# Kernel tuning notes

Hardware: AMD Instinct MI355X
Metric: run time of the kernel (lower is better)

Reference implementation:

```python
import jax, jax.numpy as jnp
import numpy as np

VOCAB, D, H, L, SEQ = 32000, 768, 12, 6, 1024
HD = D // H
DFF = 4 * D
EPS = 1e-5


def _ln(x, g, b):
    mu = jnp.mean(x, axis=-1, keepdims=True)
    var = jnp.var(x, axis=-1, keepdims=True)
    return (x - mu) * jax.lax.rsqrt(var + EPS) * g + b


def setup_inputs() -> dict:
    key = jax.random.key(0)
    ks = jax.random.split(key, 10)
    s = lambda *sh: 0.02
    return {
        "idx": jax.random.randint(ks[0], (2, SEQ), 0, VOCAB, dtype=jnp.int64) if jax.config.jax_enable_x64 else jax.random.randint(ks[0], (2, SEQ), 0, VOCAB, dtype=jnp.int32),
        "tok_emb": jax.random.normal(ks[1], (VOCAB, D), jnp.float32) * 0.02,
        "pos_emb": jax.random.normal(ks[2], (SEQ, D), jnp.float32) * 0.02,
        "Wqkv": jax.random.normal(ks[3], (L, D, 3 * D), jnp.float32) * 0.02,
        "bqkv": jnp.zeros((L, 3 * D), jnp.float32),
        "Wo": jax.random.normal(ks[4], (L, D, D), jnp.float32) * 0.02,
        "bo": jnp.zeros((L, D), jnp.float32),
        "ln1_g": jnp.ones((L, D), jnp.float32),
        "ln1_b": jnp.zeros((L, D), jnp.float32),
        "ln2_g": jnp.ones((L, D), jnp.float32),
        "ln2_b": jnp.zeros((L, D), jnp.float32),
        "W1": jax.random.normal(ks[5], (L, D, DFF), jnp.float32) * 0.02,
        "b1": jnp.zeros((L, DFF), jnp.float32),
        "W2": jax.random.normal(ks[6], (L, DFF, D), jnp.float32) * 0.02,
        "b2": jnp.zeros((L, D), jnp.float32),
        "lnf_g": jnp.ones((D,), jnp.float32),
        "lnf_b": jnp.zeros((D,), jnp.float32),
        "Wlm": jax.random.normal(ks[7], (D, VOCAB), jnp.float32) * 0.02,
    }


def _forward(idx, tok_emb, pos_emb, Wqkv, bqkv, Wo, bo, ln1_g, ln1_b,
             ln2_g, ln2_b, W1, b1, W2, b2, lnf_g, lnf_b, Wlm):
    B, T = idx.shape
    x = tok_emb[idx] + pos_emb[None, :T]  # [B,T,D]
    causal = jnp.tril(jnp.ones((T, T), bool))  # [T,T]
    for l in range(L):
        h = _ln(x, ln1_g[l], ln1_b[l])
        qkv = h @ Wqkv[l] + bqkv[l]  # [B,T,3D]
        qkv = qkv.reshape(B, T, 3, H, HD).transpose(2, 0, 3, 1, 4)
        q, k, v = qkv[0], qkv[1], qkv[2]  # each [B,H,T,HD]
        att = jnp.einsum('bhqd,bhkd->bhqk', q, k) / np.sqrt(HD).astype(np.float32)
        att = jnp.where(causal, att, -jnp.inf)
        att = jax.nn.softmax(att, axis=-1)
        o = jnp.einsum('bhqk,bhkd->bhqd', att, v)
        o = o.transpose(0, 2, 1, 3).reshape(B, T, D)
        x = x + o @ Wo[l] + bo[l]
        h = _ln(x, ln2_g[l], ln2_b[l])
        x = x + jax.nn.gelu(h @ W1[l] + b1[l], approximate=False) @ W2[l] + b2[l]
    x = _ln(x, lnf_g, lnf_b)
    return x @ Wlm  # [B,T,VOCAB]


def reference(idx, tok_emb, pos_emb, Wqkv, bqkv, Wo, bo, ln1_g, ln1_b,
              ln2_g, ln2_b, W1, b1, W2, b2, lnf_g, lnf_b, Wlm):
    return _forward(idx, tok_emb, pos_emb, Wqkv, bqkv, Wo, bo, ln1_g, ln1_b,
                    ln2_g, ln2_b, W1, b1, W2, b2, lnf_g, lnf_b, Wlm)
```

## Files before the change

### kernel.cpp

```cpp
#include <hip/hip_runtime.h>
#include <math.h>

#define TT   1024
#define DD   768
#define HH   12
#define LLAY 6
#define DFFN 3072
#define BB   2
#define NTOK (BB*TT)

typedef __bf16 bf16;
typedef __attribute__((ext_vector_type(8))) __bf16 bf16x8;
typedef __attribute__((ext_vector_type(4))) __bf16 bf16x4;
typedef __attribute__((ext_vector_type(4))) float f32x4;

__device__ inline unsigned pack_bf16x2(float a, float b) {
    union { bf16 h[2]; unsigned u; } un;
    un.h[0] = (bf16)a; un.h[1] = (bf16)b;
    return un.u;
}

__device__ inline void gload16(const bf16* g, bf16* l) {
    __builtin_amdgcn_global_load_lds((const void*)g, (void*)l, 16, 0, 0);
}

template<int N> __device__ inline void waitcnt_vm() {
    if constexpr (N == 0) asm volatile("s_waitcnt vmcnt(0)" ::: "memory");
    else if constexpr (N == 3) asm volatile("s_waitcnt vmcnt(3)" ::: "memory");
    else if constexpr (N == 4) asm volatile("s_waitcnt vmcnt(4)" ::: "memory");
}

__global__ __launch_bounds__(256) void embed_kernel(const int* __restrict__ idx,
                                                    const float* __restrict__ tok,
                                                    const float* __restrict__ pos,
                                                    float* __restrict__ x) {
    int bt = blockIdx.x;
    int t  = bt % TT;
    int id = idx[bt];
    const float* te = tok + (size_t)id * DD;
    const float* pe = pos + (size_t)t * DD;
    float* xr = x + (size_t)bt * DD;
    for (int d = threadIdx.x; d < DD; d += 256) xr[d] = te[d] + pe[d];
}

__global__ __launch_bounds__(256) void ln_kernel(const float* __restrict__ in,
                                                 const float* __restrict__ g,
                                                 const float* __restrict__ b,
                                                 bf16* __restrict__ out) {
    int row = blockIdx.x;
    const float* xr = in + (size_t)row * DD;
    float s = 0.f, s2 = 0.f;
    for (int d = threadIdx.x; d < DD; d += 256) { float v = xr[d]; s += v; s2 += v * v; }
    for (int off = 32; off; off >>= 1) { s += __shfl_down(s, off); s2 += __shfl_down(s2, off); }
    __shared__ float aS[4], aS2[4];
    __shared__ float mu_s, rs_s;
    int wid = threadIdx.x >> 6, lane = threadIdx.x & 63;
    if (lane == 0) { aS[wid] = s; aS2[wid] = s2; }
    __syncthreads();
    if (threadIdx.x == 0) {
        float t1 = aS[0] + aS[1] + aS[2] + aS[3];
        float t2 = aS2[0] + aS2[1] + aS2[2] + aS2[3];
        float mu = t1 / (float)DD;
        float var = t2 / (float)DD - mu * mu;
        mu_s = mu; rs_s = rsqrtf(var + 1e-5f);
    }
    __syncthreads();
    float mu = mu_s, rs = rs_s;
    bf16* orow = out + (size_t)row * DD;
    for (int d = threadIdx.x; d < DD; d += 256)
        orow[d] = (bf16)((xr[d] - mu) * rs * g[d] + b[d]);
}

__device__ inline void convT_tile(const float* __restrict__ in, bf16* __restrict__ out,
                                  int K, int N, int k0, int n0) {
    __shared__ float tile[32][33];
    int tn = threadIdx.x & 31, tk = threadIdx.x >> 5;
#pragma unroll
    for (int i = 0; i < 4; ++i)
        tile[tk + i * 8][tn] = in[(size_t)(k0 + tk + i * 8) * N + n0 + tn];
    __syncthreads();
#pragma unroll
    for (int i = 0; i < 4; ++i)
        out[(size_t)(n0 + tk + i * 8) * K + k0 + tn] = (bf16)tile[tn][tk + i * 8];
}

__global__ __launch_bounds__(256) void convT_kernel(const float* __restrict__ in,
                                                    bf16* __restrict__ out,
                                                    int K, int N) {
    convT_tile(in, out, K, N, blockIdx.y * 32, blockIdx.x * 32);
}

__global__ __launch_bounds__(256) void convT4_kernel(const float* __restrict__ w0,
                                                     const float* __restrict__ w1,
                                                     const float* __restrict__ w2,
                                                     const float* __restrict__ w3,
                                                     bf16* __restrict__ o0,
                                                     bf16* __restrict__ o1,
                                                     bf16* __restrict__ o2,
                                                     bf16* __restrict__ o3) {
    int bid = blockIdx.x;
    const float* in; bf16* out; int K, N, t;
    if (bid < 1728)      { in = w0; out = o0; K = 768;  N = 2304; t = bid; }
    else if (bid < 2304) { in = w1; out = o1; K = 768;  N = 768;  t = bid - 1728; }
    else if (bid < 4608) { in = w2; out = o2; K = 768;  N = 3072; t = bid - 2304; }
    else                 { in = w3; out = o3; K = 3072; N = 768;  t = bid - 4608; }
    int nt = N / 32;
    convT_tile(in, out, K, N, (t / nt) * 32, (t % nt) * 32);
}

template<int BM, int EPI>
__global__ __launch_bounds__(256) void mgemm(const bf16* __restrict__ A,
                                             const bf16* __restrict__ Bt,
                                             const float* __restrict__ bias,
                                             const float* __restrict__ res,
                                             void* __restrict__ Cout,
                                             bf16* __restrict__ vtout,
                                             int M, int N, int K) {
    constexpr int MF = BM / 32;
    constexpr int NF = 4;
    constexpr int AIT = BM / 64;
    constexpr int STG = AIT + 2;
    constexpr int ASZ = BM * 32;
    constexpr int BUFE = ASZ + 128 * 32;
    __shared__ __align__(16) bf16 smem[3 * BUFE];
    int bm = (EPI == 0 ? blockIdx.x : blockIdx.y) * BM;
    int bn = (EPI == 0 ? blockIdx.y : blockIdx.x) * 128;
    int tid = threadIdx.x;
    int lane = tid & 63;
    int w = tid >> 6;
    int wr = w >> 1, wc = w & 1;
    int l15 = lane & 15, g = lane >> 4;

    f32x4 acc[MF][NF];
#pragma unroll
    for (int m = 0; m < MF; ++m)
#pragma unroll
        for (int n = 0; n < NF; ++n) acc[m][n] = (f32x4){0.f, 0.f, 0.f, 0.f};

    int r = lane >> 2;
    int koff = ((lane & 3) ^ ((r >> 1) & 3)) * 8;
    const bf16* Ab = A + (size_t)(bm + w * 16 + r) * K + koff;
    const bf16* Bb = Bt + (size_t)(bn + w * 16 + r) * K + koff;

    auto stage = [&](int p, int k0) {
        bf16* base = smem + p * BUFE;
        bf16* Asb = base + w * 16 * 32;
        bf16* Bsb = base + ASZ + w * 16 * 32;
#pragma unroll
        for (int it = 0; it < AIT; ++it)
            gload16(Ab + (size_t)(it * 64) * K + k0, Asb + it * 64 * 32);
#pragma unroll
        for (int it = 0; it < 2; ++it)
            gload16(Bb + (size_t)(it * 64) * K + k0, Bsb + it * 64 * 32);
    };

    stage(0, 0);
    stage(1, 32);
    waitcnt_vm<STG>();
    __builtin_amdgcn_s_barrier();
    int cur = 0;

    for (int k0 = 0; k0 < K; k0 += 32) {
        const bf16* Ac = smem + cur * BUFE;
        const bf16* Bc = Ac + ASZ;
        bf16x8 af[MF], bfv[NF];
#pragma unroll
        for (int m = 0; m < MF; ++m) {
            int row = wr * (BM / 2) + m * 16 + l15;
            int gs = g ^ ((row >> 1) & 3);
            af[m] = *(const bf16x8*)&Ac[row * 32 + gs * 8];
        }
#pragma unroll
        for (int n = 0; n < NF; ++n) {
            int row = wc * 64 + n * 16 + l15;
            int gs = g ^ ((row >> 1) & 3);
            bfv[n] = *(const bf16x8*)&Bc[row * 32 + gs * 8];
        }
        bool st = (k0 + 64 < K);
        if (st) {
            int nxt = cur + 2; if (nxt >= 3) nxt -= 3;
            stage(nxt, k0 + 64);
        }
#pragma unroll
        for (int m = 0; m < MF; ++m)
#pragma unroll
            for (int n = 0; n < NF; ++n)
                acc[m][n] = __builtin_amdgcn_mfma_f32_16x16x32_bf16(af[m], bfv[n], acc[m][n], 0, 0, 0);
        if (st) waitcnt_vm<STG>();
        else    waitcnt_vm<0>();
        __builtin_amdgcn_s_barrier();
        cur = (cur == 2) ? 0 : cur + 1;
    }

    int lq = g * 4;
    if (EPI == 0) {
        float* elds = (float*)smem;
        float* eb = &elds[w * 16 * 68];
        int rr = lane >> 2, c0 = (lane & 3) * 16;
#pragma unroll
        for (int mf = 0; mf < MF; ++mf) {
#pragma unroll
            for (int n = 0; n < NF; ++n)
#pragma unroll
                for (int j = 0; j < 4; ++j)
                    eb[(lq + j) * 68 + n * 16 + l15] = acc[mf][n][j];
            __syncthreads();
            const float* src = &eb[rr * 68 + c0];
            float* dst = (float*)Cout + (size_t)(bm + wr * 64 + mf * 16 + rr) * N + bn + wc * 64 + c0;
            *(float4*)(dst + 0)  = *(const float4*)(src + 0);
            *(float4*)(dst + 4)  = *(const float4*)(src + 4);
            *(float4*)(dst + 8)  = *(const float4*)(src + 8);
            *(float4*)(dst + 12) = *(const float4*)(src + 12);
            __syncthreads();
        }
        return;
    }

#pragma unroll
    for (int m = 0; m < MF; ++m) {
#pragma unroll
        for (int n = 0; n < NF; ++n) {
            int col = bn + wc * 64 + n * 16 + l15;
            float bv = (EPI >= 1) ? bias[col] : 0.f;
            if (EPI == 4 && col >= 2 * DD) {
                int row0 = bm + wr * (BM / 2) + m * 16 + lq;
                int b = row0 >> 10, t0 = row0 & 1023;
                int hd = col - 2 * DD;
                union { bf16 h[4]; unsigned long long u; } pk;
#pragma unroll
                for (int j = 0; j < 4; ++j) pk.h[j] = (bf16)(acc[m][n][j] + bv);
                *(unsigned long long*)&vtout[((size_t)(b * DD + hd)) * TT + t0] = pk.u;
            } else {
#pragma unroll
                for (int j = 0; j < 4; ++j) {
                    int row = bm + wr * (BM / 2) + m * 16 + lq + j;
                    float v = acc[m][n][j] + bv;
                    if (EPI == 2) {
                        ((float*)Cout)[(size_t)row * N + col] = v + res[(size_t)row * N + col];
                    } else if (EPI == 3) {
                        v = 0.5f * v * (1.f + erff(v * 0.70710678118654752f));
                        ((bf16*)Cout)[(size_t)row * N + col] = (bf16)v;
                    } else if (EPI == 1) {
                        ((bf16*)Cout)[(size_t)row * N + col] = (bf16)v;
                    } else {
                        if (col < DD) v *= 0.125f;
                        ((bf16*)Cout)[(size_t)row * N + col] = (bf16)v;
                    }
                }
            }
        }
    }
}

__global__ __launch_bounds__(256) void fattn_kernel(const bf16* __restrict__ qkv,
                                                    const bf16* __restrict__ vt,
                                                    bf16* __restrict__ o) {
    const int bh = blockIdx.y;
    const int b = bh / HH, h = bh % HH;
    const int q0 = blockIdx.x * 64;
    const int tid = threadIdx.x;
    const int w = tid >> 6, lane = tid & 63;
    const int l15 = lane & 15, g = lane >> 4;

    __shared__ __align__(16) bf16 Ks[64 * 64];
    __shared__ __align__(16) bf16 Vs[64 * 64];
    __shared__ __align__(16) bf16 Ps[4][16 * 64];

    const size_t basebt = (size_t)b * TT;
    const int qw = q0 + w * 16;
    const int qg = qw + l15;

    bf16x8 bq0, bq1;
    {
        const bf16* qp = qkv + (basebt + qw + l15) * 2304 + h * 64 + g * 8;
        bq0 = *(const bf16x8*)(qp);
        bq1 = *(const bf16x8*)(qp + 32);
    }

    float mstate = -1e30f, lstate = 0.f;
    f32x4 oacc[4];
#pragma unroll
    for (int nf = 0; nf < 4; ++nf) oacc[nf] = (f32x4){0.f, 0.f, 0.f, 0.f};

    const int swzA = (l15 & 7) << 4;
    char* const psBase = (char*)&Ps[w][0];

    const int nchunk = blockIdx.x + 1;
    for (int c = 0; c < nchunk; ++c) {
        const int kc = c * 64;
        __syncthreads();
        {
            int r0 = tid >> 3;
            int e0 = (tid & 7) * 8;
#pragma unroll
            for (int i = 0; i < 2; ++i) {
                int r = r0 + 32 * i;
                int swzW = (r & 7) << 4;
                bf16x8 kv = *(const bf16x8*)&qkv[(basebt + kc + r) * 2304 + DD + h * 64 + e0];
                *(bf16x8*)((char*)Ks + r * 128 + ((e0 * 2) ^ swzW)) = kv;
                bf16x8 vv = *(const bf16x8*)&vt[((size_t)bh * 64 + r) * TT + kc + e0];
                *(bf16x8*)((char*)Vs + r * 128 + ((e0 * 2) ^ swzW)) = vv;
            }
        }
        __syncthreads();
        if (kc > qw + 15) continue;

        f32x4 s[4];
        __builtin_amdgcn_s_setprio(1);
#pragma unroll
        for (int mf = 0; mf < 4; ++mf) {
            char* kr = (char*)Ks + (16 * mf + l15) * 128;
            bf16x8 ka0 = *(const bf16x8*)(kr + ((16 * g) ^ swzA));
            bf16x8 ka1 = *(const bf16x8*)(kr + ((64 + 16 * g) ^ swzA));
            f32x4 a = (f32x4){0.f, 0.f, 0.f, 0.f};
            a = __builtin_amdgcn_mfma_f32_16x16x32_bf16(ka0, bq0, a, 0, 0, 0);
            a = __builtin_amdgcn_mfma_f32_16x16x32_bf16(ka1, bq1, a, 0, 0, 0);
            s[mf] = a;
        }
        __builtin_amdgcn_s_setprio(0);
        if (kc + 63 > qw) {
#pragma unroll
            for (int mf = 0; mf < 4; ++mf)
#pragma unroll
                for (int j = 0; j < 4; ++j)
                    if (kc + 16 * mf + 4 * g + j > qg) s[mf][j] = -1e30f;
        }
        float cm = -1e30f;
#pragma unroll
        for (int mf = 0; mf < 4; ++mf)
#pragma unroll
            for (int j = 0; j < 4; ++j) cm = fmaxf(cm, s[mf][j]);
        cm = fmaxf(cm, __shfl_xor(cm, 16));
        cm = fmaxf(cm, __shfl_xor(cm, 32));
        float mnew = fmaxf(mstate, cm);
        float sc = __expf(mstate - mnew);
        mstate = mnew;
        float p[4][4];
        float psum = 0.f;
#pragma unroll
        for (int mf = 0; mf < 4; ++mf)
#pragma unroll
            for (int j = 0; j < 4; ++j) { float pv = __expf(s[mf][j] - mnew); p[mf][j] = pv; psum += pv; }
        psum += __shfl_xor(psum, 16);
        psum += __shfl_xor(psum, 32);
        lstate = lstate * sc + psum;
#pragma unroll
        for (int mf = 0; mf < 4; ++mf) {
            unsigned lo = pack_bf16x2(p[mf][0], p[mf][1]);
            unsigned hi = pack_bf16x2(p[mf][2], p[mf][3]);
            char* dst = psBase + l15 * 128 + ((32 * mf + 8 * g) ^ swzA);
            *(unsigned*)dst = lo;
            *(unsigned*)(dst + 4) = hi;
        }
        float s0 = __shfl(sc, 4 * g + 0), s1 = __shfl(sc, 4 * g + 1);
        float s2 = __shfl(sc, 4 * g + 2), s3 = __shfl(sc, 4 * g + 3);
#pragma unroll
        for (int nf = 0; nf < 4; ++nf) {
            oacc[nf][0] *= s0; oacc[nf][1] *= s1; oacc[nf][2] *= s2; oacc[nf][3] *= s3;
        }
        bf16x8 pa0 = *(const bf16x8*)(psBase + l15 * 128 + ((16 * g) ^ swzA));
        bf16x8 pa1 = *(const bf16x8*)(psBase + l15 * 128 + ((64 + 16 * g) ^ swzA));
        __builtin_amdgcn_s_setprio(1);
#pragma unroll
        for (int nf = 0; nf < 4; ++nf) {
            char* vr = (char*)Vs + (16 * nf + l15) * 128;
            bf16x8 vb0 = *(const bf16x8*)(vr + ((16 * g) ^ swzA));
            bf16x8 vb1 = *(const bf16x8*)(vr + ((64 + 16 * g) ^ swzA));
            oacc[nf] = __builtin_amdgcn_mfma_f32_16x16x32_bf16(pa0, vb0, oacc[nf], 0, 0, 0);
            oacc[nf] = __builtin_amdgcn_mfma_f32_16x16x32_bf16(pa1, vb1, oacc[nf], 0, 0, 0);
        }
        __builtin_amdgcn_s_setprio(0);
    }
    float linv = 1.f / lstate;
    float l0 = __shfl(linv, 4 * g + 0), l1 = __shfl(linv, 4 * g + 1);
    float l2 = __shfl(linv, 4 * g + 2), l3 = __shfl(linv, 4 * g + 3);
    float lj[4] = {l0, l1, l2, l3};
#pragma unroll
    for (int j = 0; j < 4; ++j) {
        bf16* orow = o + (size_t)(basebt + qw + 4 * g + j) * DD + h * 64 + l15;
#pragma unroll
        for (int nf = 0; nf < 4; ++nf)
            orow[16 * nf] = (bf16)(oacc[nf][j] * lj[j]);
    }
}

extern "C" void kernel_launch(void* const* d_in, const int* in_sizes, int n_in,
                              void* d_out, int out_size, void* d_ws, size_t ws_size,
                              hipStream_t stream) {
    (void)in_sizes; (void)n_in; (void)out_size; (void)ws_size;
    const int*   idx  = (const int*)d_in[0];
    const float* tok  = (const float*)d_in[1];
    const float* pos  = (const float*)d_in[2];
    const float* Wqkv = (const float*)d_in[3];
    const float* bqkv = (const float*)d_in[4];
    const float* Wo   = (const float*)d_in[5];
    const float* bo   = (const float*)d_in[6];
    const float* ln1g = (const float*)d_in[7];
    const float* ln1b = (const float*)d_in[8];
    const float* ln2g = (const float*)d_in[9];
    const float* ln2b = (const float*)d_in[10];
    const float* W1   = (const float*)d_in[11];
    const float* b1   = (const float*)d_in[12];
    const float* W2   = (const float*)d_in[13];
    const float* b2   = (const float*)d_in[14];
    const float* lnfg = (const float*)d_in[15];
    const float* lnfb = (const float*)d_in[16];
    const float* Wlm  = (const float*)d_in[17];
    float* out = (float*)d_out;

    char* ws = (char*)d_ws;
    float* x     = (float*)(ws);
    bf16*  abuf0 = (bf16*)(ws + 6291456);
    bf16*  abuf1 = (bf16*)(ws + 9437184);
    bf16*  qkvb  = (bf16*)(ws + 22020096);
    bf16*  vtb   = (bf16*)(ws + 31457280);
    bf16*  wbuf  = (bf16*)(ws + 34603008);

    bf16* wq = wbuf;
    bf16* wo = wbuf + 1769472;
    bf16* w1 = wbuf + 2359296;
    bf16* w2 = wbuf + 4718592;

    embed_kernel<<<NTOK, 256, 0, stream>>>(idx, tok, pos, x);

    for (int l = 0; l < LLAY; ++l) {
        convT4_kernel<<<6912, 256, 0, stream>>>(
            Wqkv + (size_t)l * DD * 3 * DD, Wo + (size_t)l * DD * DD,
            W1 + (size_t)l * DD * DFFN, W2 + (size_t)l * DFFN * DD,
            wq, wo, w1, w2);
        ln_kernel<<<NTOK, 256, 0, stream>>>(x, ln1g + l * DD, ln1b + l * DD, abuf0);
        mgemm<128, 4><<<dim3(3 * DD / 128, NTOK / 128), 256, 0, stream>>>(
            abuf0, wq, bqkv + (size_t)l * 3 * DD, nullptr, qkvb, vtb, NTOK, 3 * DD, DD);
        fattn_kernel<<<dim3(TT / 64, BB * HH), 256, 0, stream>>>(qkvb, vtb, abuf0);
        mgemm<64, 2><<<dim3(DD / 128, NTOK / 64), 256, 0, stream>>>(
            abuf0, wo, bo + (size_t)l * DD, x, x, nullptr, NTOK, DD, DD);
        ln_kernel<<<NTOK, 256, 0, stream>>>(x, ln2g + l * DD, ln2b + l * DD, abuf0);
        mgemm<128, 3><<<dim3(DFFN / 128, NTOK / 128), 256, 0, stream>>>(
            abuf0, w1, b1 + (size_t)l * DFFN, nullptr, abuf1, nullptr, NTOK, DFFN, DD);
        mgemm<64, 2><<<dim3(DD / 128, NTOK / 64), 256, 0, stream>>>(
            abuf1, w2, b2 + (size_t)l * DD, x, x, nullptr, NTOK, DD, DFFN);
    }
    ln_kernel<<<NTOK, 256, 0, stream>>>(x, lnfg, lnfb, abuf0);
    convT_kernel<<<dim3(32000 / 32, DD / 32), 256, 0, stream>>>(Wlm, wbuf, DD, 32000);
    mgemm<128, 0><<<dim3(NTOK / 128, 32000 / 128), 256, 0, stream>>>(
        abuf0, wbuf, nullptr, nullptr, out, nullptr, NTOK, 32000, DD);
}
```

Baseline: 1.024 ms.

## Add dedicated 256x256-tile LM-head GEMM kernel with double-buffered LDS

Replaces the generic mgemm used for the vocabulary projection with a specialized 512-thread kernel. It computes 256x256 output tiles, stages K in 64-wide double-buffered swizzled LDS tiles, and splits the B-tile loads around the MFMA bursts, using s_setprio to favour the MFMA issue. The larger tiles are meant to raise operand reuse and cut global/LDS traffic for the largest GEMM. In exchange, the 128KB of LDS per block limits occupancy, and the kernel hardcodes K=768 and N=32000. The generic kernel's EPI==0 path is dropped.

```diff
diff --git a/kernel.cpp b/kernel.cpp
--- a/kernel.cpp
+++ b/kernel.cpp
@@ -123,8 +123,8 @@
     constexpr int ASZ = BM * 32;
     constexpr int BUFE = ASZ + 128 * 32;
     __shared__ __align__(16) bf16 smem[3 * BUFE];
-    int bm = (EPI == 0 ? blockIdx.x : blockIdx.y) * BM;
-    int bn = (EPI == 0 ? blockIdx.y : blockIdx.x) * 128;
+    int bm = blockIdx.y * BM;
+    int bn = blockIdx.x * 128;
     int tid = threadIdx.x;
     int lane = tid & 63;
     int w = tid >> 6;
@@ -193,35 +193,12 @@
     }
 
     int lq = g * 4;
-    if (EPI == 0) {
-        float* elds = (float*)smem;
-        float* eb = &elds[w * 16 * 68];
-        int rr = lane >> 2, c0 = (lane & 3) * 16;
-#pragma unroll
-        for (int mf = 0; mf < MF; ++mf) {
-#pragma unroll
-            for (int n = 0; n < NF; ++n)
-#pragma unroll
-                for (int j = 0; j < 4; ++j)
-                    eb[(lq + j) * 68 + n * 16 + l15] = acc[mf][n][j];
-            __syncthreads();
-            const float* src = &eb[rr * 68 + c0];
-            float* dst = (float*)Cout + (size_t)(bm + wr * 64 + mf * 16 + rr) * N + bn + wc * 64 + c0;
-            *(float4*)(dst + 0)  = *(const float4*)(src + 0);
-            *(float4*)(dst + 4)  = *(const float4*)(src + 4);
-            *(float4*)(dst + 8)  = *(const float4*)(src + 8);
-            *(float4*)(dst + 12) = *(const float4*)(src + 12);
-            __syncthreads();
-        }
-        return;
-    }
-
 #pragma unroll
     for (int m = 0; m < MF; ++m) {
 #pragma unroll
         for (int n = 0; n < NF; ++n) {
             int col = bn + wc * 64 + n * 16 + l15;
-            float bv = (EPI >= 1) ? bias[col] : 0.f;
+            float bv = bias[col];
             if (EPI == 4 && col >= 2 * DD) {
                 int row0 = bm + wr * (BM / 2) + m * 16 + lq;
                 int b = row0 >> 10, t0 = row0 & 1023;
@@ -249,6 +226,115 @@
                 }
             }
         }
+    }
+}
+
+__global__ __launch_bounds__(512, 2) void lmgemm(const bf16* __restrict__ A,
+                                                 const bf16* __restrict__ Bt,
+                                                 float* __restrict__ C) {
+    constexpr int BUFE = 2 * 256 * 64;
+    __shared__ __align__(16) bf16 smem[2 * BUFE];
+    const int tid = threadIdx.x;
+    const int w = tid >> 6, lane = tid & 63;
+    const int wm = w >> 2, wn = w & 3;
+    const int l15 = lane & 15, g = lane >> 4;
+    const int bm = blockIdx.x * 256;
+    const int bn = blockIdx.y * 256;
+
+    const int swzr = (l15 >> 1) & 7;
+    const int pc0 = (g ^ swzr) * 8;
+
+    const int r8 = lane >> 3, c8 = lane & 7;
+    const bf16* agp[4]; const bf16* bgp[4];
+    int aldso[4], bldso[4];
+#pragma unroll
+    for (int j = 0; j < 4; ++j) {
+        int br = w * 32 + j * 8 + r8;
+        int swz = (br >> 1) & 7;
+        agp[j] = A  + (size_t)(bm + br) * DD + (c8 ^ swz) * 8;
+        bgp[j] = Bt + (size_t)(bn + br) * DD + (c8 ^ swz) * 8;
+        aldso[j] = (w * 32 + j * 8) * 64;
+        bldso[j] = 256 * 64 + (w * 32 + j * 8) * 64;
+    }
+
+    f32x4 acc[8][4];
+#pragma unroll
+    for (int m = 0; m < 8; ++m)
+#pragma unroll
+        for (int n = 0; n < 4; ++n) acc[m][n] = (f32x4){0.f, 0.f, 0.f, 0.f};
+
+    {
+        bf16* base = smem;
+#pragma unroll
+        for (int j = 0; j < 4; ++j) gload16(agp[j], base + aldso[j]);
+#pragma unroll
+        for (int j = 0; j < 4; ++j) gload16(bgp[j], base + bldso[j]);
+    }
+    __syncthreads();
+    int cur = 0;
+
+    for (int t = 0; t < 12; ++t) {
+        const bf16* Ar = smem + cur * BUFE;
+        const bf16* Br = Ar + 256 * 64;
+        bf16* nbase = smem + (cur ^ 1) * BUFE;
+        const int k0n = (t + 1) * 64;
+        const bool st = (t < 11);
+        if (st) {
+#pragma unroll
+            for (int j = 0; j < 4; ++j) gload16(agp[j] + k0n, nbase + aldso[j]);
+        }
+        bf16x8 af[8], bfv[4];
+#pragma unroll
+        for (int m = 0; m < 8; ++m)
+            af[m] = *(const bf16x8*)&Ar[(wm * 128 + m * 16 + l15) * 64 + pc0];
+#pragma unroll
+        for (int n = 0; n < 4; ++n)
+            bfv[n] = *(const bf16x8*)&Br[(wn * 64 + n * 16 + l15) * 64 + pc0];
+        __builtin_amdgcn_s_setprio(1);
+#pragma unroll
+        for (int m = 0; m < 8; ++m)
+#pragma unroll
+            for (int n = 0; n < 4; ++n)
+                acc[m][n] = __builtin_amdgcn_mfma_f32_16x16x32_bf16(af[m], bfv[n], acc[m][n], 0, 0, 0);
+        __builtin_amdgcn_s_setprio(0);
+        if (st) {
+#pragma unroll
+            for (int j = 0; j < 4; ++j) gload16(bgp[j] + k0n, nbase + bldso[j]);
+        }
+#pragma unroll
+        for (int m = 0; m < 8; ++m)
+            af[m] = *(const bf16x8*)&Ar[(wm * 128 + m * 16 + l15) * 64 + (pc0 ^ 32)];
+#pragma unroll
+        for (int n = 0; n < 4; ++n)
+            bfv[n] = *(const bf16x8*)&Br[(wn * 64 + n * 16 + l15) * 64 + (pc0 ^ 32)];
+        __builtin_amdgcn_s_setprio(1);
+#pragma unroll
+        for (int m = 0; m < 8; ++m)
+#pragma unroll
+            for (int n = 0; n < 4; ++n)
+                acc[m][n] = __builtin_amdgcn_mfma_f32_16x16x32_bf16(af[m], bfv[n], acc[m][n], 0, 0, 0);
+        __builtin_amdgcn_s_setprio(0);
+        __syncthreads();
+        cur ^= 1;
+    }
+
+    float* eb = (float*)smem + w * (16 * 68);
+    const int rr = lane >> 2, c0 = (lane & 3) * 16;
+#pragma unroll
+    for (int mf = 0; mf < 8; ++mf) {
+#pragma unroll
+        for (int n = 0; n < 4; ++n)
+#pragma unroll
+            for (int j = 0; j < 4; ++j)
+                eb[(g * 4 + j) * 68 + n * 16 + l15] = acc[mf][n][j];
+        __syncthreads();
+        const float* src = &eb[rr * 68 + c0];
+        float* dst = C + (size_t)(bm + wm * 128 + mf * 16 + rr) * 32000 + bn + wn * 64 + c0;
+        *(float4*)(dst + 0)  = *(const float4*)(src + 0);
+        *(float4*)(dst + 4)  = *(const float4*)(src + 4);
+        *(float4*)(dst + 8)  = *(const float4*)(src + 8);
+        *(float4*)(dst + 12) = *(const float4*)(src + 12);
+        __syncthreads();
     }
 }
 
@@ -442,6 +528,5 @@
     }
     ln_kernel<<<NTOK, 256, 0, stream>>>(x, lnfg, lnfb, abuf0);
     convT_kernel<<<dim3(32000 / 32, DD / 32), 256, 0, stream>>>(Wlm, wbuf, DD, 32000);
-    mgemm<128, 0><<<dim3(NTOK / 128, 32000 / 128), 256, 0, stream>>>(
-        abuf0, wbuf, nullptr, nullptr, out, nullptr, NTOK, 32000, DD);
-}
+    lmgemm<<<dim3(NTOK / 256, 32000 / 256), 512, 0, stream>>>(abuf0, wbuf, out);
+}
```

After: 1.008 ms. No clear change (-1.5%).
